# Optimization experiments

Hardware: AMD Instinct MI355X
Metric: run time of the kernel (lower is better)

The kernel has to match this reference:

```python
import jax, jax.numpy as jnp
import numpy as np

BSZ, T, L, D = 8, 8, 196, 192
E = D            # expand=1 -> d_inner
C = E * T        # d_inner_s = d_inner * d_t (scan channels)
N = 16           # d_state
K = 4            # d_conv
R = 96           # dt_rank = ceil(d_model*d_t/16)
DT_MIN, DT_MAX, DT_FLOOR = 1e-3, 1e-1, 1e-4


def setup_inputs() -> dict:
    key = jax.random.key(0)
    ks = jax.random.split(key, 9)
    hidden = jax.random.normal(ks[0], (BSZ, T, L, D), jnp.float32)
    in_proj_w = jax.random.normal(ks[1], (2 * E, D), jnp.float32) * (D ** -0.5)
    conv_w = jax.random.normal(ks[2], (C, K), jnp.float32) * 0.2
    conv_b = jax.random.normal(ks[3], (C,), jnp.float32) * 0.05
    x_proj_w = jax.random.normal(ks[4], (R + 2 * N, C), jnp.float32) * (C ** -0.5)
    dt_init_std = R ** -0.5
    dt_proj_w = jax.random.uniform(ks[5], (C, R), jnp.float32, -dt_init_std, dt_init_std)
    dt = jnp.exp(jax.random.uniform(ks[6], (C,), jnp.float32) * (np.log(DT_MAX) - np.log(DT_MIN)) + np.log(DT_MIN))
    dt = jnp.clip(dt, DT_FLOOR)
    dt_bias = dt + jnp.log(-jnp.expm1(-dt))  # inverse-softplus init
    A_log = jnp.log(jnp.tile(jnp.arange(1, N + 1, dtype=jnp.float32), (C, 1)))
    D_param = jnp.ones((C,), jnp.float32)
    return {"hidden": hidden, "in_proj_w": in_proj_w, "conv_w": conv_w, "conv_b": conv_b,
            "x_proj_w": x_proj_w, "dt_proj_w": dt_proj_w, "dt_bias": dt_bias,
            "A_log": A_log, "D_param": D_param}


def _silu(x):
    return x * jax.nn.sigmoid(x)


def reference(hidden, in_proj_w, conv_w, conv_b, x_proj_w, dt_proj_w, dt_bias, A_log, D_param):
    Bsz, T_, L_, D_ = hidden.shape
    E_ = in_proj_w.shape[0] // 2
    # in_proj (no bias): (B,T,L,D) @ (2E,D)^T -> (B,2E,T,L)
    xz = jnp.einsum('btld,ed->betl', hidden, in_proj_w)
    # rearrange 'b d t l -> b (d t) l' then chunk(2, dim=1)
    x = xz[:, :E_].reshape(Bsz, E_ * T_, L_)   # (B, C, L)
    z = xz[:, E_:].reshape(Bsz, E_ * T_, L_)
    # causal depthwise conv1d + silu
    x = jax.lax.conv_general_dilated(
        x, conv_w[:, None, :], window_strides=(1,), padding=[(K - 1, 0)],
        dimension_numbers=('NCH', 'OIH', 'NCH'), feature_group_count=conv_w.shape[0])
    x = _silu(x + conv_b[None, :, None])
    # x_proj -> dt, B, C
    x_dbl = jnp.einsum('bcl,rc->brl', x, x_proj_w)  # (B, R+2N, L)
    dt = x_dbl[:, :R]
    B_ssm = x_dbl[:, R:R + N]        # (B, N, L)
    C_ssm = x_dbl[:, R + N:]         # (B, N, L)
    delta = jax.nn.softplus(jnp.einsum('brl,cr->bcl', dt, dt_proj_w) + dt_bias[None, :, None])
    A = -jnp.exp(A_log)              # (C, N)
    # selective scan: h_l = exp(delta*A) * h_{l-1} + delta*B*x
    dA = jnp.exp(jnp.einsum('bcl,cn->lbcn', delta, A))       # (L,B,C,N)
    dBu = jnp.einsum('bcl,bnl,bcl->lbcn', delta, B_ssm, x)   # (L,B,C,N)

    def step(h, ab):
        a, b = ab
        h = h * a + b
        return h, h

    h0 = jnp.zeros((Bsz, dA.shape[2], dA.shape[3]), x.dtype)
    _, hs = jax.lax.scan(step, h0, (dA, dBu))                # (L,B,C,N)
    y = jnp.einsum('lbcn,bnl->bcl', hs, C_ssm)
    y = y + x * D_param[None, :, None]
    out = y * _silu(z)               # (B, C, L) — fused path output before out_proj
    return out
```

## Files before the change

### kernel.cpp

```cpp
#include <hip/hip_runtime.h>
#include <hip/hip_bf16.h>
#include <cstddef>

#define BSZ 8
#define T_  8
#define L_  196
#define D_  192
#define E_  192
#define C_  1536
#define N_  16
#define K_  4
#define R_  96

typedef __attribute__((ext_vector_type(8))) short short8;
typedef __attribute__((ext_vector_type(4))) float f32x4;
typedef unsigned short ushort_t;

__device__ __forceinline__ ushort_t f2bf(float x) {
  unsigned int bits = __float_as_uint(x);
  bits += 0x7FFFu + ((bits >> 16) & 1u);
  return (ushort_t)(bits >> 16);
}

__global__ __launch_bounds__(256) void k_cast_all(
    const float* __restrict__ hidden, const float* __restrict__ w,
    const float* __restrict__ wdt,
    ushort_t* __restrict__ hb, ushort_t* __restrict__ wb,
    ushort_t* __restrict__ wdtb) {
  const int H8 = 301056;
  const int W8 = H8 + 9216;
  const int T8 = W8 + 18432;
  int i = blockIdx.x * 256 + threadIdx.x;
  if (i >= T8) return;
  const float4* ip; uint4* op; int j;
  if (i < H8)      { ip = (const float4*)hidden; op = (uint4*)hb;   j = i; }
  else if (i < W8) { ip = (const float4*)w;      op = (uint4*)wb;   j = i - H8; }
  else             { ip = (const float4*)wdt;    op = (uint4*)wdtb; j = i - W8; }
  float4 v0 = ip[(size_t)j * 2];
  float4 v1 = ip[(size_t)j * 2 + 1];
  union { ushort_t u[8]; uint4 v; } r;
  float f[8] = {v0.x, v0.y, v0.z, v0.w, v1.x, v1.y, v1.z, v1.w};
#pragma unroll
  for (int k = 0; k < 8; k++) r.u[k] = f2bf(f[k]);
  op[j] = r.v;
}

__global__ __launch_bounds__(256) void k_inproj_mfma(
    const ushort_t* __restrict__ hb, const ushort_t* __restrict__ wb,
    float* __restrict__ xb, float* __restrict__ zb) {
  __shared__ float smem[64][97];
  int tid = threadIdx.x;
  int wave = tid >> 6, lane = tid & 63;
  int m0b = blockIdx.x * 64;
  int n0 = blockIdx.y * 96;
  int row = lane & 15, kg = lane >> 4;
  int m0w = m0b + wave * 16;

  f32x4 acc[6] = {};
  const ushort_t* ap = hb + (size_t)(m0w + row) * 192 + kg * 8;
#pragma unroll
  for (int ks = 0; ks < 6; ks++) {
    short8 a = *(const short8*)(ap + ks * 32);
#pragma unroll
    for (int nt = 0; nt < 6; nt++) {
      short8 b = *(const short8*)(wb + (size_t)(n0 + nt * 16 + row) * 192 + ks * 32 + kg * 8);
      acc[nt] = __builtin_amdgcn_mfma_f32_16x16x32_bf16(a, b, acc[nt], 0, 0, 0);
    }
  }
#pragma unroll
  for (int nt = 0; nt < 6; nt++) {
#pragma unroll
    for (int j = 0; j < 4; j++) {
      smem[wave * 16 + kg * 4 + j][nt * 16 + row] = acc[nt][j];
    }
  }
  __syncthreads();
  int mloc = tid & 63, eof = tid >> 6;
  int m_glob = m0b + mloc;
  int b = m_glob / 1568, u = m_glob % 1568;
  size_t obase = (size_t)b * 301056 + u;
#pragma unroll
  for (int e = eof; e < 96; e += 4) {
    int eg = n0 + e;
    float v = smem[mloc][e];
    if (eg < 192) xb[obase + (size_t)eg * 1568] = v;
    else          zb[obase + (size_t)(eg - 192) * 1568] = v;
  }
}

__global__ __launch_bounds__(256) void k_inproj_f32(
    const float* __restrict__ A, const float* __restrict__ W,
    float* __restrict__ xb, float* __restrict__ zb) {
  __shared__ float As[16][132];
  __shared__ float Bs[16][132];
  int tid = threadIdx.x;
  int m0 = blockIdx.x * 128;
  int n0 = blockIdx.y * 128;
  int tx = tid & 15, ty = tid >> 4;
  float acc[8][8] = {};
  for (int k0 = 0; k0 < 192; k0 += 16) {
#pragma unroll
    for (int i = 0; i < 2; i++) {
      int idx = tid + i * 256;
      int m = idx >> 2, k4 = (idx & 3) * 4;
      float4 v = *(const float4*)&A[(size_t)(m0 + m) * 192 + k0 + k4];
      As[k4 + 0][m] = v.x; As[k4 + 1][m] = v.y;
      As[k4 + 2][m] = v.z; As[k4 + 3][m] = v.w;
    }
#pragma unroll
    for (int i = 0; i < 2; i++) {
      int idx = tid + i * 256;
      int n = idx >> 2, k4 = (idx & 3) * 4;
      float4 v = *(const float4*)&W[(size_t)(n0 + n) * 192 + k0 + k4];
      Bs[k4 + 0][n] = v.x; Bs[k4 + 1][n] = v.y;
      Bs[k4 + 2][n] = v.z; Bs[k4 + 3][n] = v.w;
    }
    __syncthreads();
#pragma unroll
    for (int kk = 0; kk < 16; kk++) {
      float a_[8], b_[8];
      *(float4*)&a_[0] = *(const float4*)&As[kk][ty * 4];
      *(float4*)&a_[4] = *(const float4*)&As[kk][ty * 4 + 64];
      *(float4*)&b_[0] = *(const float4*)&Bs[kk][tx * 4];
      *(float4*)&b_[4] = *(const float4*)&Bs[kk][tx * 4 + 64];
#pragma unroll
      for (int i = 0; i < 8; i++)
#pragma unroll
        for (int j = 0; j < 8; j++) acc[i][j] += a_[i] * b_[j];
    }
    __syncthreads();
  }
#pragma unroll
  for (int i = 0; i < 8; i++) {
    int m = m0 + ty * 4 + (i & 3) + ((i >> 2) * 64);
    int b = m / (T_ * L_);
    int r = m % (T_ * L_);
    int t = r / L_;
    int l = r % L_;
#pragma unroll
    for (int j = 0; j < 8; j++) {
      int e = n0 + tx * 4 + (j & 3) + ((j >> 2) * 64);
      float v = acc[i][j];
      if (e < E_) {
        int c = e * T_ + t;
        xb[((size_t)b * C_ + c) * L_ + l] = v;
      } else {
        int c = (e - E_) * T_ + t;
        zb[((size_t)b * C_ + c) * L_ + l] = v;
      }
    }
  }
}

__global__ __launch_bounds__(256) void k_conv(
    const float* __restrict__ xb, const float* __restrict__ conv_w,
    const float* __restrict__ conv_b, float* __restrict__ xc) {
  int idx = blockIdx.x * 256 + threadIdx.x;
  int l = idx % L_;
  int bc = idx / L_;
  int c = bc % C_;
  const float* xrow = xb + (size_t)bc * L_;
  const float* w = conv_w + c * K_;
  float acc = conv_b[c];
#pragma unroll
  for (int k = 0; k < K_; k++) {
    int ll = l - (K_ - 1) + k;
    if (ll >= 0) acc += xrow[ll] * w[k];
  }
  xc[idx] = acc / (1.f + __expf(-acc));
}

#define XKK 32
__global__ __launch_bounds__(256) void k_xdbl_tile(
    const float* __restrict__ xb, const float* __restrict__ conv_w,
    const float* __restrict__ conv_b, const float* __restrict__ W,
    float* __restrict__ part, float* __restrict__ xcout) {
  __shared__ float Ws2[XKK][132];
  __shared__ float Xs[XKK][64];
  int tid = threadIdx.x;
  int n0 = blockIdx.x * 64;
  int c0 = blockIdx.y * 96;
  int tx = tid & 15, ty = tid >> 4;
  float acc[8][4] = {};
  for (int ck = 0; ck < 96; ck += XKK) {
#pragma unroll
    for (int p = 0; p < 4; p++) {
      int idx = tid + p * 256;
      int r = idx >> 3;
      int c4 = (idx & 7) * 4;
      float4 w4 = *(const float4*)&W[(size_t)r * 1536 + c0 + ck + c4];
      Ws2[c4 + 0][r] = w4.x; Ws2[c4 + 1][r] = w4.y;
      Ws2[c4 + 2][r] = w4.z; Ws2[c4 + 3][r] = w4.w;
    }
#pragma unroll
    for (int p = 0; p < 8; p++) {
      int idx = tid + p * 256;
      int c = idx >> 6, j = idx & 63;
      int n = n0 + j;
      float v = 0.f;
      if (n < BSZ * L_) {
        int b = n / L_, l = n - b * L_;
        int cc = c0 + ck + c;
        const float* row = xb + ((size_t)b * C_ + cc) * L_;
        float s = conv_b[cc];
#pragma unroll
        for (int k = 0; k < K_; k++) {
          int ll = l - 3 + k;
          if (ll >= 0) s += row[ll] * conv_w[cc * K_ + k];
        }
        v = s / (1.f + __expf(-s));
        xcout[((size_t)b * C_ + cc) * L_ + l] = v;
      }
      Xs[c][j] = v;
    }
    __syncthreads();
#pragma unroll
    for (int kk = 0; kk < XKK; kk++) {
      float w_[8], x_[4];
      *(float4*)&w_[0] = *(const float4*)&Ws2[kk][ty * 8];
      *(float4*)&w_[4] = *(const float4*)&Ws2[kk][ty * 8 + 4];
      *(float4*)&x_[0] = *(const float4*)&Xs[kk][tx * 4];
#pragma unroll
      for (int i = 0; i < 8; i++)
#pragma unroll
        for (int j = 0; j < 4; j++) acc[i][j] += w_[i] * x_[j];
    }
    __syncthreads();
  }
  int kc = blockIdx.y;
#pragma unroll
  for (int j = 0; j < 4; j++) {
    int n = n0 + tx * 4 + j;
    if (n < BSZ * L_) {
      int b = n / L_, l = n - b * L_;
      float* pp = &part[(((size_t)kc * 8 + b) * L_ + l) * 128 + ty * 8];
      float4 v0 = {acc[0][j], acc[1][j], acc[2][j], acc[3][j]};
      float4 v1 = {acc[4][j], acc[5][j], acc[6][j], acc[7][j]};
      *(float4*)&pp[0] = v0;
      *(float4*)&pp[4] = v1;
    }
  }
}

__global__ __launch_bounds__(256) void k_xreduce(
    const float* __restrict__ part, ushort_t* __restrict__ dtt,
    float* __restrict__ Bt, float* __restrict__ Ct) {
  int tx = threadIdx.x & 63;
  int ty = threadIdx.x >> 6;
  int l = blockIdx.x * 4 + ty;
  int b = blockIdx.y;
  size_t o = ((size_t)b * L_ + l) * 128 + tx;
  float v0 = 0.f, v1 = 0.f;
#pragma unroll
  for (int kc = 0; kc < 16; kc++) {
    v0 += part[(size_t)kc * (8 * L_ * 128) + o];
    v1 += part[(size_t)kc * (8 * L_ * 128) + o + 64];
  }
  int r1 = tx + 64;
  size_t nrow = ((size_t)b * L_ + l) * 96;
  dtt[nrow + tx] = f2bf(v0);
  if (r1 < 96) {
    dtt[nrow + r1] = f2bf(v1);
  } else if (r1 < 96 + N_) {
    Bt[((size_t)b * L_ + l) * N_ + (r1 - 96)] = v1;
  } else {
    Ct[((size_t)b * L_ + l) * N_ + (r1 - 96 - N_)] = v1;
  }
}

__global__ __launch_bounds__(256) void k_xdbl_mono(
    const float* __restrict__ xc, const float* __restrict__ W,
    float* __restrict__ xdbl, float* __restrict__ Bt, float* __restrict__ Ct) {
  int tx = threadIdx.x & 63;
  int ty = threadIdx.x >> 6;
  int l = blockIdx.x * 64 + tx;
  int r0 = blockIdx.y * 4 + ty;
  int r1 = r0 + 64;
  int b = blockIdx.z;
  if (l >= L_) return;
  const float* xcb = xc + (size_t)b * C_ * L_;
  float acc0 = 0.f, acc1 = 0.f;
#pragma unroll 4
  for (int c = 0; c < C_; c++) {
    float v = xcb[(size_t)c * L_ + l];
    acc0 += v * W[(size_t)r0 * C_ + c];
    acc1 += v * W[(size_t)r1 * C_ + c];
  }
  xdbl[((size_t)b * 96 + r0) * L_ + l] = acc0;
  if (r1 < 96) {
    xdbl[((size_t)b * 96 + r1) * L_ + l] = acc1;
  } else if (r1 < 96 + N_) {
    Bt[((size_t)b * L_ + l) * N_ + (r1 - 96)] = acc1;
  } else {
    Ct[((size_t)b * L_ + l) * N_ + (r1 - 96 - N_)] = acc1;
  }
}

__global__ __launch_bounds__(256) void k_delta_mfma(
    const ushort_t* __restrict__ wdtb,
    const ushort_t* __restrict__ dtt,
    const float* __restrict__ dt_bias, float* __restrict__ delta) {
  __shared__ float smem[64][65];
  int tid = threadIdx.x;
  int wave = tid >> 6, lane = tid & 63;
  int n0 = blockIdx.x * 64;
  int c0b = blockIdx.y * 64;
  int row = lane & 15, kg = lane >> 4;
  int c0w = c0b + wave * 16;
  f32x4 acc[4] = {};
  const ushort_t* ap = wdtb + (size_t)(c0w + row) * 96 + kg * 8;
#pragma unroll
  for (int ks = 0; ks < 3; ks++) {
    short8 a = *(const short8*)(ap + ks * 32);
#pragma unroll
    for (int nt = 0; nt < 4; nt++) {
      short8 b = *(const short8*)(dtt + (size_t)(n0 + nt * 16 + row) * 96 + ks * 32 + kg * 8);
      acc[nt] = __builtin_amdgcn_mfma_f32_16x16x32_bf16(a, b, acc[nt], 0, 0, 0);
    }
  }
#pragma unroll
  for (int nt = 0; nt < 4; nt++)
#pragma unroll
    for (int j = 0; j < 4; j++)
      smem[wave * 16 + kg * 4 + j][nt * 16 + row] = acc[nt][j];
  __syncthreads();
  int c_loc = tid >> 2, q = tid & 3;
  int c = c0b + c_loc;
  float bias = dt_bias[c];
#pragma unroll
  for (int i = 0; i < 16; i++) {
    int nn = n0 + q * 16 + i;
    if (nn < BSZ * L_) {
      int b = nn / L_, l = nn - b * L_;
      float v = smem[c_loc][q * 16 + i] + bias;
      float sp = (v > 20.f) ? v : __logf(1.f + __expf(v));
      delta[((size_t)b * C_ + c) * L_ + l] = sp;
    }
  }
}

__global__ __launch_bounds__(256) void k_delta_gemm(
    const float* __restrict__ dtm, const float* __restrict__ Wdt,
    const float* __restrict__ dt_bias, float* __restrict__ delta) {
  __shared__ float Ws[96][68];
  __shared__ float Ds[96][68];
  int tid = threadIdx.x;
  int n0 = blockIdx.x * 64;
  int c0 = blockIdx.y * 64;
  for (int idx = tid; idx < 64 * 96; idx += 256) {
    int i = idx / 96, r = idx - i * 96;
    Ws[r][i] = Wdt[(size_t)(c0 + i) * 96 + r];
  }
  for (int idx = tid; idx < 96 * 64; idx += 256) {
    int r = idx >> 6, j = idx & 63;
    int n = n0 + j;
    float v = 0.f;
    if (n < BSZ * L_) {
      int b = n / L_, l = n - b * L_;
      v = dtm[((size_t)b * 96 + r) * L_ + l];
    }
    Ds[r][j] = v;
  }
  __syncthreads();
  int tx = tid & 15, ty = tid >> 4;
  float acc[4][4] = {};
#pragma unroll 8
  for (int r = 0; r < 96; r++) {
    float4 av = *(const float4*)&Ws[r][ty * 4];
    float4 bv = *(const float4*)&Ds[r][tx * 4];
    float a_[4] = {av.x, av.y, av.z, av.w};
    float b_[4] = {bv.x, bv.y, bv.z, bv.w};
#pragma unroll
    for (int i = 0; i < 4; i++)
#pragma unroll
      for (int j = 0; j < 4; j++) acc[i][j] += a_[i] * b_[j];
  }
#pragma unroll
  for (int i = 0; i < 4; i++) {
    int c = c0 + ty * 4 + i;
    float bias = dt_bias[c];
#pragma unroll
    for (int j = 0; j < 4; j++) {
      int n = n0 + tx * 4 + j;
      if (n < BSZ * L_) {
        int b = n / L_, l = n - b * L_;
        float v = acc[i][j] + bias;
        float sp = (v > 20.f) ? v : __logf(1.f + __expf(v));
        delta[((size_t)b * C_ + c) * L_ + l] = sp;
      }
    }
  }
}

__global__ __launch_bounds__(512) void k_scan_fused(
    const float* __restrict__ delta, const float* __restrict__ xc,
    const float* __restrict__ zb, const float* __restrict__ Bt,
    const float* __restrict__ Ct, const float* __restrict__ A_log,
    const float* __restrict__ D_param, float* __restrict__ out) {
  __shared__ float BtS[196][20];
  __shared__ float CtS[196][20];
  __shared__ float yS[16][196];
  int tid = threadIdx.x;
  int b = blockIdx.y;
  int c_base = blockIdx.x * 16;
  int wave = tid >> 6, lane = tid & 63;
  int chunk = lane & 15;
  int nl = lane >> 4;
  bool act = chunk < 14;
  const int l0 = chunk * 14;
  int c0 = c_base + wave * 2;
  int c1 = c0 + 1;

  {
    const float4* gB = (const float4*)(Bt + (size_t)b * L_ * N_);
    const float4* gC = (const float4*)(Ct + (size_t)b * L_ * N_);
    for (int i = tid; i < 784; i += 512) {
      int l = i >> 2, q = i & 3;
      *(float4*)&BtS[l][q * 4] = gB[i];
      *(float4*)&CtS[l][q * 4] = gC[i];
    }
  }

  float4 a0, a1;
  {
    float4 t0 = *(const float4*)&A_log[c0 * N_ + nl * 4];
    float4 t1 = *(const float4*)&A_log[c1 * N_ + nl * 4];
    a0.x = -__expf(t0.x); a0.y = -__expf(t0.y);
    a0.z = -__expf(t0.z); a0.w = -__expf(t0.w);
    a1.x = -__expf(t1.x); a1.y = -__expf(t1.y);
    a1.z = -__expf(t1.z); a1.w = -__expf(t1.w);
  }
  size_t w0 = (size_t)(b * C_ + c0) * L_ + l0;
  size_t w1 = (size_t)(b * C_ + c1) * L_ + l0;

  float2 dv0[7], xv0[7], dv1[7], xv1[7];
  if (act) {
    const float2* d2a = (const float2*)(delta + w0);
    const float2* d2b = (const float2*)(delta + w1);
    const float2* x2a = (const float2*)(xc + w0);
    const float2* x2b = (const float2*)(xc + w1);
#pragma unroll
    for (int i = 0; i < 7; i++) {
      dv0[i] = d2a[i]; dv1[i] = d2b[i];
      xv0[i] = x2a[i]; xv1[i] = x2b[i];
    }
  } else {
#pragma unroll
    for (int i = 0; i < 7; i++) {
      dv0[i] = {0.f, 0.f}; dv1[i] = {0.f, 0.f};
      xv0[i] = {0.f, 0.f}; xv1[i] = {0.f, 0.f};
    }
  }
  __syncthreads();

  float4 h0 = {0.f,0.f,0.f,0.f}, p0 = {1.f,1.f,1.f,1.f};
  float4 h1 = {0.f,0.f,0.f,0.f}, p1 = {1.f,1.f,1.f,1.f};
#pragma unroll
  for (int l = 0; l < 14; l++) {
    float d0 = (l & 1) ? dv0[l >> 1].y : dv0[l >> 1].x;
    float d1 = (l & 1) ? dv1[l >> 1].y : dv1[l >> 1].x;
    float x0 = (l & 1) ? xv0[l >> 1].y : xv0[l >> 1].x;
    float x1 = (l & 1) ? xv1[l >> 1].y : xv1[l >> 1].x;
    float du0 = d0 * x0, du1 = d1 * x1;
    float4 Bv = *(const float4*)&BtS[l0 + l][nl * 4];
    float e0x = __expf(d0 * a0.x), e0y = __expf(d0 * a0.y);
    float e0z = __expf(d0 * a0.z), e0w = __expf(d0 * a0.w);
    float e1x = __expf(d1 * a1.x), e1y = __expf(d1 * a1.y);
    float e1z = __expf(d1 * a1.z), e1w = __expf(d1 * a1.w);
    h0.x = h0.x * e0x + du0 * Bv.x; p0.x *= e0x;
    h0.y = h0.y * e0y + du0 * Bv.y; p0.y *= e0y;
    h0.z = h0.z * e0z + du0 * Bv.z; p0.z *= e0z;
    h0.w = h0.w * e0w + du0 * Bv.w; p0.w *= e0w;
    h1.x = h1.x * e1x + du1 * Bv.x; p1.x *= e1x;
    h1.y = h1.y * e1y + du1 * Bv.y; p1.y *= e1y;
    h1.z = h1.z * e1z + du1 * Bv.z; p1.z *= e1z;
    h1.w = h1.w * e1w + du1 * Bv.w; p1.w *= e1w;
  }

#pragma unroll
  for (int s = 1; s < 16; s <<= 1) {
    float4 P0, Q0, P1, Q1;
    P0.x = __shfl_up(p0.x, s, 16); Q0.x = __shfl_up(h0.x, s, 16);
    P0.y = __shfl_up(p0.y, s, 16); Q0.y = __shfl_up(h0.y, s, 16);
    P0.z = __shfl_up(p0.z, s, 16); Q0.z = __shfl_up(h0.z, s, 16);
    P0.w = __shfl_up(p0.w, s, 16); Q0.w = __shfl_up(h0.w, s, 16);
    P1.x = __shfl_up(p1.x, s, 16); Q1.x = __shfl_up(h1.x, s, 16);
    P1.y = __shfl_up(p1.y, s, 16); Q1.y = __shfl_up(h1.y, s, 16);
    P1.z = __shfl_up(p1.z, s, 16); Q1.z = __shfl_up(h1.z, s, 16);
    P1.w = __shfl_up(p1.w, s, 16); Q1.w = __shfl_up(h1.w, s, 16);
    if (chunk >= s) {
      h0.x = p0.x * Q0.x + h0.x; p0.x *= P0.x;
      h0.y = p0.y * Q0.y + h0.y; p0.y *= P0.y;
      h0.z = p0.z * Q0.z + h0.z; p0.z *= P0.z;
      h0.w = p0.w * Q0.w + h0.w; p0.w *= P0.w;
      h1.x = p1.x * Q1.x + h1.x; p1.x *= P1.x;
      h1.y = p1.y * Q1.y + h1.y; p1.y *= P1.y;
      h1.z = p1.z * Q1.z + h1.z; p1.z *= P1.z;
      h1.w = p1.w * Q1.w + h1.w; p1.w *= P1.w;
    }
  }
  float4 g0, g1;
  g0.x = __shfl_up(h0.x, 1, 16); g1.x = __shfl_up(h1.x, 1, 16);
  g0.y = __shfl_up(h0.y, 1, 16); g1.y = __shfl_up(h1.y, 1, 16);
  g0.z = __shfl_up(h0.z, 1, 16); g1.z = __shfl_up(h1.z, 1, 16);
  g0.w = __shfl_up(h0.w, 1, 16); g1.w = __shfl_up(h1.w, 1, 16);
  if (chunk == 0) {
    g0.x = g0.y = g0.z = g0.w = 0.f;
    g1.x = g1.y = g1.z = g1.w = 0.f;
  }

  if (act) {
#pragma unroll
    for (int l = 0; l < 14; l++) {
      float d0 = (l & 1) ? dv0[l >> 1].y : dv0[l >> 1].x;
      float d1 = (l & 1) ? dv1[l >> 1].y : dv1[l >> 1].x;
      float x0 = (l & 1) ? xv0[l >> 1].y : xv0[l >> 1].x;
      float x1 = (l & 1) ? xv1[l >> 1].y : xv1[l >> 1].x;
      float du0 = d0 * x0, du1 = d1 * x1;
      float4 Bv = *(const float4*)&BtS[l0 + l][nl * 4];
      float4 Cv = *(const float4*)&CtS[l0 + l][nl * 4];
      float e0x = __expf(d0 * a0.x), e0y = __expf(d0 * a0.y);
      float e0z = __expf(d0 * a0.z), e0w = __expf(d0 * a0.w);
      float e1x = __expf(d1 * a1.x), e1y = __expf(d1 * a1.y);
      float e1z = __expf(d1 * a1.z), e1w = __expf(d1 * a1.w);
      g0.x = g0.x * e0x + du0 * Bv.x;
      g0.y = g0.y * e0y + du0 * Bv.y;
      g0.z = g0.z * e0z + du0 * Bv.z;
      g0.w = g0.w * e0w + du0 * Bv.w;
      g1.x = g1.x * e1x + du1 * Bv.x;
      g1.y = g1.y * e1y + du1 * Bv.y;
      g1.z = g1.z * e1z + du1 * Bv.z;
      g1.w = g1.w * e1w + du1 * Bv.w;
      float y0 = g0.x * Cv.x + g0.y * Cv.y + g0.z * Cv.z + g0.w * Cv.w;
      float y1 = g1.x * Cv.x + g1.y * Cv.y + g1.z * Cv.z + g1.w * Cv.w;
      y0 += __shfl_xor(y0, 16);
      y0 += __shfl_xor(y0, 32);
      y1 += __shfl_xor(y1, 16);
      y1 += __shfl_xor(y1, 32);
      if (nl == 0) {
        yS[wave * 2 + 0][l0 + l] = y0;
        yS[wave * 2 + 1][l0 + l] = y1;
      }
    }
  }
  __syncthreads();

  size_t base = (size_t)(b * C_ + c_base) * L_;
  for (int idx = tid; idx < 16 * L_; idx += 512) {
    int cloc = idx / L_, l = idx - cloc * L_;
    float y = yS[cloc][l];
    float xv = xc[base + idx];
    float zv = zb[base + idx];
    float Dp = D_param[c_base + cloc];
    float sz = zv / (1.f + __expf(-zv));
    out[base + idx] = (y + xv * Dp) * sz;
  }
}

extern "C" void kernel_launch(void* const* d_in, const int* in_sizes, int n_in,
                              void* d_out, int out_size, void* d_ws, size_t ws_size,
                              hipStream_t stream) {
  const float* hidden    = (const float*)d_in[0];
  const float* in_proj_w = (const float*)d_in[1];
  const float* conv_w    = (const float*)d_in[2];
  const float* conv_b    = (const float*)d_in[3];
  const float* x_proj_w  = (const float*)d_in[4];
  const float* dt_proj_w = (const float*)d_in[5];
  const float* dt_bias   = (const float*)d_in[6];
  const float* A_log     = (const float*)d_in[7];
  const float* D_param   = (const float*)d_in[8];
  float* out = (float*)d_out;

  const size_t NBCL   = (size_t)BSZ * C_ * L_;
  const size_t NBT    = (size_t)BSZ * L_ * N_;
  const size_t NDT    = (size_t)BSZ * 96 * L_;
  const size_t NPART  = (size_t)16 * BSZ * L_ * 128;
  const size_t NHID   = (size_t)BSZ * T_ * L_ * D_;
  const size_t NW1    = (size_t)2 * E_ * D_;
  const size_t NDTTF  = 76800;
  const size_t NWDTF  = 73728;
  float* ws = (float*)d_ws;
  float* xb    = ws;
  float* zb    = xb + NBCL;
  float* xc    = zb + NBCL;
  float* BtArr = xc + NBCL;
  float* CtArr = BtArr + NBT;
  float* dttF  = CtArr + NBT;
  float* wdtbF = dttF + NDTTF;
  float* Pbuf  = wdtbF + NWDTF;
  float* delta = xb;

  size_t need = 3 * NBCL + 2 * NBT + NDTTF + NWDTF + NPART;
  bool split_ok = ws_size / 4 >= need;

  if (split_ok) {
    ushort_t* hb   = (ushort_t*)Pbuf;
    ushort_t* wb   = hb + NHID;
    ushort_t* wdtb = (ushort_t*)wdtbF;
    ushort_t* dtt  = (ushort_t*)dttF;
    float* part = Pbuf;

    k_cast_all<<<1284, 256, 0, stream>>>(hidden, in_proj_w, dt_proj_w, hb, wb, wdtb);
    k_inproj_mfma<<<dim3(196, 4), 256, 0, stream>>>(hb, wb, xb, zb);
    k_xdbl_tile<<<dim3(25, 16), 256, 0, stream>>>(xb, conv_w, conv_b, x_proj_w, part, xc);
    k_xreduce<<<dim3(49, BSZ), 256, 0, stream>>>(part, dtt, BtArr, CtArr);
    k_delta_mfma<<<dim3(25, 24), 256, 0, stream>>>(wdtb, dtt, dt_bias, delta);
    k_scan_fused<<<dim3(C_ / 16, BSZ), 512, 0, stream>>>(delta, xc, zb, BtArr, CtArr,
                                                         A_log, D_param, out);
  } else {
    float* xdblF = Pbuf;
    k_inproj_f32<<<dim3(98, 3), 256, 0, stream>>>(hidden, in_proj_w, xb, zb);
    k_conv<<<(int)(NBCL / 256), 256, 0, stream>>>(xb, conv_w, conv_b, xc);
    k_xdbl_mono<<<dim3(4, 16, BSZ), 256, 0, stream>>>(xc, x_proj_w, xdblF, BtArr, CtArr);
    k_delta_gemm<<<dim3(25, 24), 256, 0, stream>>>(xdblF, dt_proj_w, dt_bias, delta);
    k_scan_fused<<<dim3(C_ / 16, BSZ), 512, 0, stream>>>(delta, xc, zb, BtArr, CtArr,
                                                         A_log, D_param, out);
  }
}
```

Baseline: 119.8 us.

## Replace fp32 split-K x_proj GEMM with bf16 MFMA and conv-cast kernel

Splits the fused conv+x_proj tile kernel into a conv+SiLU kernel that also writes a transposed bf16 copy of the activations, followed by a bf16 MFMA GEMM over the full 1536-wide reduction. This removes the split-K partial buffer and its separate reduction kernel, and moves the x_proj work from FP32 FMA onto matrix cores. The x_proj weight is now cast to bf16 in the existing cast kernel. The cost is an extra bf16 activation buffer and lower precision in the dt/B/C projections. The MFMA kernel launches only 200 blocks, each running a serial 48-step reduction.

```diff
diff --git a/kernel.cpp b/kernel.cpp
--- a/kernel.cpp
+++ b/kernel.cpp
@@ -24,18 +24,20 @@
 
 __global__ __launch_bounds__(256) void k_cast_all(
     const float* __restrict__ hidden, const float* __restrict__ w,
-    const float* __restrict__ wdt,
+    const float* __restrict__ wdt, const float* __restrict__ wx,
     ushort_t* __restrict__ hb, ushort_t* __restrict__ wb,
-    ushort_t* __restrict__ wdtb) {
+    ushort_t* __restrict__ wdtb, ushort_t* __restrict__ wxb) {
   const int H8 = 301056;
   const int W8 = H8 + 9216;
-  const int T8 = W8 + 18432;
+  const int D8 = W8 + 18432;
+  const int T8 = D8 + 24576;
   int i = blockIdx.x * 256 + threadIdx.x;
   if (i >= T8) return;
   const float4* ip; uint4* op; int j;
   if (i < H8)      { ip = (const float4*)hidden; op = (uint4*)hb;   j = i; }
   else if (i < W8) { ip = (const float4*)w;      op = (uint4*)wb;   j = i - H8; }
-  else             { ip = (const float4*)wdt;    op = (uint4*)wdtb; j = i - W8; }
+  else if (i < D8) { ip = (const float4*)wdt;    op = (uint4*)wdtb; j = i - W8; }
+  else             { ip = (const float4*)wx;     op = (uint4*)wxb;  j = i - D8; }
   float4 v0 = ip[(size_t)j * 2];
   float4 v1 = ip[(size_t)j * 2 + 1];
   union { ushort_t u[8]; uint4 v; } r;
@@ -152,6 +154,48 @@
   }
 }
 
+__global__ __launch_bounds__(256) void k_conv_cast(
+    const float* __restrict__ xb, const float* __restrict__ conv_w,
+    const float* __restrict__ conv_b, float* __restrict__ xc,
+    ushort_t* __restrict__ xcb) {
+  __shared__ float sm[64][33];
+  int tid = threadIdx.x;
+  int l0 = blockIdx.x * 32;
+  int c0 = blockIdx.y * 64;
+  int b  = blockIdx.z;
+  int c_loc = tid >> 2, lq = tid & 3;
+  int c = c0 + c_loc;
+  const float* xrow = xb + ((size_t)b * C_ + c) * L_;
+  float* xcrow = xc + ((size_t)b * C_ + c) * L_;
+  float w0 = conv_w[c * K_ + 0], w1 = conv_w[c * K_ + 1];
+  float w2 = conv_w[c * K_ + 2], w3 = conv_w[c * K_ + 3];
+  float cb = conv_b[c];
+#pragma unroll
+  for (int i = 0; i < 8; i++) {
+    int l = l0 + lq * 8 + i;
+    if (l < L_) {
+      float s = cb;
+      if (l >= 3) s += xrow[l - 3] * w0;
+      if (l >= 2) s += xrow[l - 2] * w1;
+      if (l >= 1) s += xrow[l - 1] * w2;
+      s += xrow[l] * w3;
+      float v = s / (1.f + __expf(-s));
+      xcrow[l] = v;
+      sm[c_loc][lq * 8 + i] = v;
+    }
+  }
+  __syncthreads();
+  int l_loc = tid >> 3, cg = tid & 7;
+  int l = l0 + l_loc;
+  if (l < L_) {
+    int n = b * L_ + l;
+    union { ushort_t u[8]; uint4 v; } r;
+#pragma unroll
+    for (int i = 0; i < 8; i++) r.u[i] = f2bf(sm[cg * 8 + i][l_loc]);
+    *(uint4*)&xcb[(size_t)n * 1536 + c0 + cg * 8] = r.v;
+  }
+}
+
 __global__ __launch_bounds__(256) void k_conv(
     const float* __restrict__ xb, const float* __restrict__ conv_w,
     const float* __restrict__ conv_b, float* __restrict__ xc) {
@@ -170,101 +214,42 @@
   xc[idx] = acc / (1.f + __expf(-acc));
 }
 
-#define XKK 32
-__global__ __launch_bounds__(256) void k_xdbl_tile(
-    const float* __restrict__ xb, const float* __restrict__ conv_w,
-    const float* __restrict__ conv_b, const float* __restrict__ W,
-    float* __restrict__ part, float* __restrict__ xcout) {
-  __shared__ float Ws2[XKK][132];
-  __shared__ float Xs[XKK][64];
+__global__ __launch_bounds__(256) void k_xdbl_mfma(
+    const ushort_t* __restrict__ wxb,
+    const ushort_t* __restrict__ xcb,
+    ushort_t* __restrict__ dtt,
+    float* __restrict__ Bt, float* __restrict__ Ct) {
+  __shared__ float sm[16][68];
   int tid = threadIdx.x;
+  int wave = tid >> 6, lane = tid & 63;
   int n0 = blockIdx.x * 64;
-  int c0 = blockIdx.y * 96;
-  int tx = tid & 15, ty = tid >> 4;
-  float acc[8][4] = {};
-  for (int ck = 0; ck < 96; ck += XKK) {
-#pragma unroll
-    for (int p = 0; p < 4; p++) {
-      int idx = tid + p * 256;
-      int r = idx >> 3;
-      int c4 = (idx & 7) * 4;
-      float4 w4 = *(const float4*)&W[(size_t)r * 1536 + c0 + ck + c4];
-      Ws2[c4 + 0][r] = w4.x; Ws2[c4 + 1][r] = w4.y;
-      Ws2[c4 + 2][r] = w4.z; Ws2[c4 + 3][r] = w4.w;
-    }
-#pragma unroll
-    for (int p = 0; p < 8; p++) {
-      int idx = tid + p * 256;
-      int c = idx >> 6, j = idx & 63;
-      int n = n0 + j;
-      float v = 0.f;
-      if (n < BSZ * L_) {
-        int b = n / L_, l = n - b * L_;
-        int cc = c0 + ck + c;
-        const float* row = xb + ((size_t)b * C_ + cc) * L_;
-        float s = conv_b[cc];
-#pragma unroll
-        for (int k = 0; k < K_; k++) {
-          int ll = l - 3 + k;
-          if (ll >= 0) s += row[ll] * conv_w[cc * K_ + k];
-        }
-        v = s / (1.f + __expf(-s));
-        xcout[((size_t)b * C_ + cc) * L_ + l] = v;
-      }
-      Xs[c][j] = v;
-    }
-    __syncthreads();
-#pragma unroll
-    for (int kk = 0; kk < XKK; kk++) {
-      float w_[8], x_[4];
-      *(float4*)&w_[0] = *(const float4*)&Ws2[kk][ty * 8];
-      *(float4*)&w_[4] = *(const float4*)&Ws2[kk][ty * 8 + 4];
-      *(float4*)&x_[0] = *(const float4*)&Xs[kk][tx * 4];
-#pragma unroll
-      for (int i = 0; i < 8; i++)
-#pragma unroll
-        for (int j = 0; j < 4; j++) acc[i][j] += w_[i] * x_[j];
-    }
-    __syncthreads();
-  }
-  int kc = blockIdx.y;
-#pragma unroll
-  for (int j = 0; j < 4; j++) {
-    int n = n0 + tx * 4 + j;
-    if (n < BSZ * L_) {
-      int b = n / L_, l = n - b * L_;
-      float* pp = &part[(((size_t)kc * 8 + b) * L_ + l) * 128 + ty * 8];
-      float4 v0 = {acc[0][j], acc[1][j], acc[2][j], acc[3][j]};
-      float4 v1 = {acc[4][j], acc[5][j], acc[6][j], acc[7][j]};
-      *(float4*)&pp[0] = v0;
-      *(float4*)&pp[4] = v1;
-    }
-  }
-}
-
-__global__ __launch_bounds__(256) void k_xreduce(
-    const float* __restrict__ part, ushort_t* __restrict__ dtt,
-    float* __restrict__ Bt, float* __restrict__ Ct) {
-  int tx = threadIdx.x & 63;
-  int ty = threadIdx.x >> 6;
-  int l = blockIdx.x * 4 + ty;
-  int b = blockIdx.y;
-  size_t o = ((size_t)b * L_ + l) * 128 + tx;
-  float v0 = 0.f, v1 = 0.f;
-#pragma unroll
-  for (int kc = 0; kc < 16; kc++) {
-    v0 += part[(size_t)kc * (8 * L_ * 128) + o];
-    v1 += part[(size_t)kc * (8 * L_ * 128) + o + 64];
-  }
-  int r1 = tx + 64;
-  size_t nrow = ((size_t)b * L_ + l) * 96;
-  dtt[nrow + tx] = f2bf(v0);
-  if (r1 < 96) {
-    dtt[nrow + r1] = f2bf(v1);
-  } else if (r1 < 96 + N_) {
-    Bt[((size_t)b * L_ + l) * N_ + (r1 - 96)] = v1;
-  } else {
-    Ct[((size_t)b * L_ + l) * N_ + (r1 - 96 - N_)] = v1;
+  int m0 = blockIdx.y * 16;
+  int row = lane & 15, kg = lane >> 4;
+  f32x4 acc = {};
+  const ushort_t* ap = wxb + (size_t)(m0 + row) * 1536 + kg * 8;
+  const ushort_t* bp = xcb + (size_t)(n0 + wave * 16 + row) * 1536 + kg * 8;
+#pragma unroll 8
+  for (int ks = 0; ks < 48; ks++) {
+    short8 a = *(const short8*)(ap + ks * 32);
+    short8 b = *(const short8*)(bp + ks * 32);
+    acc = __builtin_amdgcn_mfma_f32_16x16x32_bf16(a, b, acc, 0, 0, 0);
+  }
+#pragma unroll
+  for (int j = 0; j < 4; j++)
+    sm[kg * 4 + j][wave * 16 + row] = acc[j];
+  __syncthreads();
+  int n_loc = tid >> 2, mg = tid & 3;
+  int n = n0 + n_loc;
+  if (m0 < 96) {
+    union { ushort_t u[4]; uint2 v; } r;
+#pragma unroll
+    for (int j = 0; j < 4; j++) r.u[j] = f2bf(sm[mg * 4 + j][n_loc]);
+    *(uint2*)&dtt[(size_t)n * 96 + m0 + mg * 4] = r.v;
+  } else if (n < BSZ * L_) {
+    float4 v = {sm[mg * 4 + 0][n_loc], sm[mg * 4 + 1][n_loc],
+                sm[mg * 4 + 2][n_loc], sm[mg * 4 + 3][n_loc]};
+    float* dst = (m0 == 96) ? Bt : Ct;
+    *(float4*)&dst[(size_t)n * 16 + mg * 4] = v;
   }
 }
 
@@ -278,11 +263,11 @@
   int r1 = r0 + 64;
   int b = blockIdx.z;
   if (l >= L_) return;
-  const float* xcb = xc + (size_t)b * C_ * L_;
+  const float* xcb2 = xc + (size_t)b * C_ * L_;
   float acc0 = 0.f, acc1 = 0.f;
 #pragma unroll 4
   for (int c = 0; c < C_; c++) {
-    float v = xcb[(size_t)c * L_ + l];
+    float v = xcb2[(size_t)c * L_ + l];
     acc0 += v * W[(size_t)r0 * C_ + c];
     acc1 += v * W[(size_t)r1 * C_ + c];
   }
@@ -573,12 +558,13 @@
 
   const size_t NBCL   = (size_t)BSZ * C_ * L_;
   const size_t NBT    = (size_t)BSZ * L_ * N_;
-  const size_t NDT    = (size_t)BSZ * 96 * L_;
-  const size_t NPART  = (size_t)16 * BSZ * L_ * 128;
   const size_t NHID   = (size_t)BSZ * T_ * L_ * D_;
   const size_t NW1    = (size_t)2 * E_ * D_;
   const size_t NDTTF  = 76800;
   const size_t NWDTF  = 73728;
+  const size_t NWXF   = 98304;
+  const size_t NXCBF  = 1228800;
+  const size_t NCASTF = (NHID + NW1) / 2;
   float* ws = (float*)d_ws;
   float* xb    = ws;
   float* zb    = xb + NBCL;
@@ -587,23 +573,27 @@
   float* CtArr = BtArr + NBT;
   float* dttF  = CtArr + NBT;
   float* wdtbF = dttF + NDTTF;
-  float* Pbuf  = wdtbF + NWDTF;
+  float* wxbF  = wdtbF + NWDTF;
+  float* xcbF  = wxbF + NWXF;
+  float* Pbuf  = xcbF + NXCBF;
   float* delta = xb;
 
-  size_t need = 3 * NBCL + 2 * NBT + NDTTF + NWDTF + NPART;
+  size_t need = 3 * NBCL + 2 * NBT + NDTTF + NWDTF + NWXF + NXCBF + NCASTF;
   bool split_ok = ws_size / 4 >= need;
 
   if (split_ok) {
     ushort_t* hb   = (ushort_t*)Pbuf;
     ushort_t* wb   = hb + NHID;
     ushort_t* wdtb = (ushort_t*)wdtbF;
+    ushort_t* wxb  = (ushort_t*)wxbF;
     ushort_t* dtt  = (ushort_t*)dttF;
-    float* part = Pbuf;
-
-    k_cast_all<<<1284, 256, 0, stream>>>(hidden, in_proj_w, dt_proj_w, hb, wb, wdtb);
+    ushort_t* xcb  = (ushort_t*)xcbF;
+
+    k_cast_all<<<1380, 256, 0, stream>>>(hidden, in_proj_w, dt_proj_w, x_proj_w,
+                                         hb, wb, wdtb, wxb);
     k_inproj_mfma<<<dim3(196, 4), 256, 0, stream>>>(hb, wb, xb, zb);
-    k_xdbl_tile<<<dim3(25, 16), 256, 0, stream>>>(xb, conv_w, conv_b, x_proj_w, part, xc);
-    k_xreduce<<<dim3(49, BSZ), 256, 0, stream>>>(part, dtt, BtArr, CtArr);
+    k_conv_cast<<<dim3(7, 24, BSZ), 256, 0, stream>>>(xb, conv_w, conv_b, xc, xcb);
+    k_xdbl_mfma<<<dim3(25, 8), 256, 0, stream>>>(wxb, xcb, dtt, BtArr, CtArr);
     k_delta_mfma<<<dim3(25, 24), 256, 0, stream>>>(wdtb, dtt, dt_bias, delta);
     k_scan_fused<<<dim3(C_ / 16, BSZ), 512, 0, stream>>>(delta, xc, zb, BtArr, CtArr,
                                                          A_log, D_param, out);
```

Result: slower. 133.5 us (+11.4%).

## Fuse dt_proj MFMA GEMM and softplus into scan kernel via shared memory

Applied to the files above, without the earlier changes.

Removes the separate delta GEMM kernel and computes delta for each scan block's 16 channels inside the scan kernel with bf16 MFMA, storing the softplus result in shared memory. This avoids writing and re-reading the full B*C*L delta tensor through global memory and saves one launch. The price is extra shared memory and MFMA work at the start of the scan kernel, which may lower occupancy. The fallback path keeps the old behaviour in a copied kernel, k_scan_f32.

```diff
diff --git a/kernel.cpp b/kernel.cpp
--- a/kernel.cpp
+++ b/kernel.cpp
@@ -296,49 +296,6 @@
   }
 }
 
-__global__ __launch_bounds__(256) void k_delta_mfma(
-    const ushort_t* __restrict__ wdtb,
-    const ushort_t* __restrict__ dtt,
-    const float* __restrict__ dt_bias, float* __restrict__ delta) {
-  __shared__ float smem[64][65];
-  int tid = threadIdx.x;
-  int wave = tid >> 6, lane = tid & 63;
-  int n0 = blockIdx.x * 64;
-  int c0b = blockIdx.y * 64;
-  int row = lane & 15, kg = lane >> 4;
-  int c0w = c0b + wave * 16;
-  f32x4 acc[4] = {};
-  const ushort_t* ap = wdtb + (size_t)(c0w + row) * 96 + kg * 8;
-#pragma unroll
-  for (int ks = 0; ks < 3; ks++) {
-    short8 a = *(const short8*)(ap + ks * 32);
-#pragma unroll
-    for (int nt = 0; nt < 4; nt++) {
-      short8 b = *(const short8*)(dtt + (size_t)(n0 + nt * 16 + row) * 96 + ks * 32 + kg * 8);
-      acc[nt] = __builtin_amdgcn_mfma_f32_16x16x32_bf16(a, b, acc[nt], 0, 0, 0);
-    }
-  }
-#pragma unroll
-  for (int nt = 0; nt < 4; nt++)
-#pragma unroll
-    for (int j = 0; j < 4; j++)
-      smem[wave * 16 + kg * 4 + j][nt * 16 + row] = acc[nt][j];
-  __syncthreads();
-  int c_loc = tid >> 2, q = tid & 3;
-  int c = c0b + c_loc;
-  float bias = dt_bias[c];
-#pragma unroll
-  for (int i = 0; i < 16; i++) {
-    int nn = n0 + q * 16 + i;
-    if (nn < BSZ * L_) {
-      int b = nn / L_, l = nn - b * L_;
-      float v = smem[c_loc][q * 16 + i] + bias;
-      float sp = (v > 20.f) ? v : __logf(1.f + __expf(v));
-      delta[((size_t)b * C_ + c) * L_ + l] = sp;
-    }
-  }
-}
-
 __global__ __launch_bounds__(256) void k_delta_gemm(
     const float* __restrict__ dtm, const float* __restrict__ Wdt,
     const float* __restrict__ dt_bias, float* __restrict__ delta) {
@@ -393,13 +350,16 @@
 }
 
 __global__ __launch_bounds__(512) void k_scan_fused(
-    const float* __restrict__ delta, const float* __restrict__ xc,
-    const float* __restrict__ zb, const float* __restrict__ Bt,
-    const float* __restrict__ Ct, const float* __restrict__ A_log,
-    const float* __restrict__ D_param, float* __restrict__ out) {
+    const float* __restrict__ xc, const float* __restrict__ zb,
+    const float* __restrict__ Bt, const float* __restrict__ Ct,
+    const float* __restrict__ A_log, const float* __restrict__ D_param,
+    const ushort_t* __restrict__ wdtb,
+    const ushort_t* __restrict__ dtt,
+    const float* __restrict__ dt_bias, float* __restrict__ out) {
   __shared__ float BtS[196][20];
   __shared__ float CtS[196][20];
   __shared__ float yS[16][196];
+  __shared__ float dS[16][200];
   int tid = threadIdx.x;
   int b = blockIdx.y;
   int c_base = blockIdx.x * 16;
@@ -421,6 +381,29 @@
     }
   }
 
+  {
+    const ushort_t* ap2 = wdtb + (size_t)(c_base + chunk) * 96 + nl * 8;
+    for (int nt = wave; nt < 13; nt += 8) {
+      f32x4 accd = {};
+      const ushort_t* bp2 = dtt + (size_t)(b * L_ + nt * 16 + chunk) * 96 + nl * 8;
+#pragma unroll
+      for (int ks = 0; ks < 3; ks++) {
+        short8 a = *(const short8*)(ap2 + ks * 32);
+        short8 bb = *(const short8*)(bp2 + ks * 32);
+        accd = __builtin_amdgcn_mfma_f32_16x16x32_bf16(a, bb, accd, 0, 0, 0);
+      }
+      int lcol = nt * 16 + chunk;
+#pragma unroll
+      for (int j = 0; j < 4; j++) {
+        int c_loc = nl * 4 + j;
+        if (lcol < L_) {
+          float v = accd[j] + dt_bias[c_base + c_loc];
+          dS[c_loc][lcol] = (v > 20.f) ? v : __logf(1.f + __expf(v));
+        }
+      }
+    }
+  }
+
   float4 a0, a1;
   {
     float4 t0 = *(const float4*)&A_log[c0 * N_ + nl * 4];
@@ -433,25 +416,29 @@
   size_t w0 = (size_t)(b * C_ + c0) * L_ + l0;
   size_t w1 = (size_t)(b * C_ + c1) * L_ + l0;
 
-  float2 dv0[7], xv0[7], dv1[7], xv1[7];
+  float2 xv0[7], xv1[7];
   if (act) {
-    const float2* d2a = (const float2*)(delta + w0);
-    const float2* d2b = (const float2*)(delta + w1);
     const float2* x2a = (const float2*)(xc + w0);
     const float2* x2b = (const float2*)(xc + w1);
 #pragma unroll
+    for (int i = 0; i < 7; i++) { xv0[i] = x2a[i]; xv1[i] = x2b[i]; }
+  } else {
+#pragma unroll
+    for (int i = 0; i < 7; i++) { xv0[i] = {0.f, 0.f}; xv1[i] = {0.f, 0.f}; }
+  }
+  __syncthreads();
+
+  float2 dv0[7], dv1[7];
+  if (act) {
+#pragma unroll
     for (int i = 0; i < 7; i++) {
-      dv0[i] = d2a[i]; dv1[i] = d2b[i];
-      xv0[i] = x2a[i]; xv1[i] = x2b[i];
+      dv0[i] = *(const float2*)&dS[wave * 2 + 0][l0 + 2 * i];
+      dv1[i] = *(const float2*)&dS[wave * 2 + 1][l0 + 2 * i];
     }
   } else {
 #pragma unroll
-    for (int i = 0; i < 7; i++) {
-      dv0[i] = {0.f, 0.f}; dv1[i] = {0.f, 0.f};
-      xv0[i] = {0.f, 0.f}; xv1[i] = {0.f, 0.f};
-    }
-  }
-  __syncthreads();
+    for (int i = 0; i < 7; i++) { dv0[i] = {0.f, 0.f}; dv1[i] = {0.f, 0.f}; }
+  }
 
   float4 h0 = {0.f,0.f,0.f,0.f}, p0 = {1.f,1.f,1.f,1.f};
   float4 h1 = {0.f,0.f,0.f,0.f}, p1 = {1.f,1.f,1.f,1.f};
@@ -557,6 +544,164 @@
   }
 }
 
+__global__ __launch_bounds__(512) void k_scan_f32(
+    const float* __restrict__ delta, const float* __restrict__ xc,
+    const float* __restrict__ zb, const float* __restrict__ Bt,
+    const float* __restrict__ Ct, const float* __restrict__ A_log,
+    const float* __restrict__ D_param, float* __restrict__ out) {
+  __shared__ float BtS[196][20];
+  __shared__ float CtS[196][20];
+  __shared__ float yS[16][196];
+  int tid = threadIdx.x;
+  int b = blockIdx.y;
+  int c_base = blockIdx.x * 16;
+  int wave = tid >> 6, lane = tid & 63;
+  int chunk = lane & 15;
+  int nl = lane >> 4;
+  bool act = chunk < 14;
+  const int l0 = chunk * 14;
+  int c0 = c_base + wave * 2;
+  int c1 = c0 + 1;
+  {
+    const float4* gB = (const float4*)(Bt + (size_t)b * L_ * N_);
+    const float4* gC = (const float4*)(Ct + (size_t)b * L_ * N_);
+    for (int i = tid; i < 784; i += 512) {
+      int l = i >> 2, q = i & 3;
+      *(float4*)&BtS[l][q * 4] = gB[i];
+      *(float4*)&CtS[l][q * 4] = gC[i];
+    }
+  }
+  float4 a0, a1;
+  {
+    float4 t0 = *(const float4*)&A_log[c0 * N_ + nl * 4];
+    float4 t1 = *(const float4*)&A_log[c1 * N_ + nl * 4];
+    a0.x = -__expf(t0.x); a0.y = -__expf(t0.y);
+    a0.z = -__expf(t0.z); a0.w = -__expf(t0.w);
+    a1.x = -__expf(t1.x); a1.y = -__expf(t1.y);
+    a1.z = -__expf(t1.z); a1.w = -__expf(t1.w);
+  }
+  size_t w0 = (size_t)(b * C_ + c0) * L_ + l0;
+  size_t w1 = (size_t)(b * C_ + c1) * L_ + l0;
+  float2 dv0[7], xv0[7], dv1[7], xv1[7];
+  if (act) {
+    const float2* d2a = (const float2*)(delta + w0);
+    const float2* d2b = (const float2*)(delta + w1);
+    const float2* x2a = (const float2*)(xc + w0);
+    const float2* x2b = (const float2*)(xc + w1);
+#pragma unroll
+    for (int i = 0; i < 7; i++) {
+      dv0[i] = d2a[i]; dv1[i] = d2b[i];
+      xv0[i] = x2a[i]; xv1[i] = x2b[i];
+    }
+  } else {
+#pragma unroll
+    for (int i = 0; i < 7; i++) {
+      dv0[i] = {0.f, 0.f}; dv1[i] = {0.f, 0.f};
+      xv0[i] = {0.f, 0.f}; xv1[i] = {0.f, 0.f};
+    }
+  }
+  __syncthreads();
+  float4 h0 = {0.f,0.f,0.f,0.f}, p0 = {1.f,1.f,1.f,1.f};
+  float4 h1 = {0.f,0.f,0.f,0.f}, p1 = {1.f,1.f,1.f,1.f};
+#pragma unroll
+  for (int l = 0; l < 14; l++) {
+    float d0 = (l & 1) ? dv0[l >> 1].y : dv0[l >> 1].x;
+    float d1 = (l & 1) ? dv1[l >> 1].y : dv1[l >> 1].x;
+    float x0 = (l & 1) ? xv0[l >> 1].y : xv0[l >> 1].x;
+    float x1 = (l & 1) ? xv1[l >> 1].y : xv1[l >> 1].x;
+    float du0 = d0 * x0, du1 = d1 * x1;
+    float4 Bv = *(const float4*)&BtS[l0 + l][nl * 4];
+    float e0x = __expf(d0 * a0.x), e0y = __expf(d0 * a0.y);
+    float e0z = __expf(d0 * a0.z), e0w = __expf(d0 * a0.w);
+    float e1x = __expf(d1 * a1.x), e1y = __expf(d1 * a1.y);
+    float e1z = __expf(d1 * a1.z), e1w = __expf(d1 * a1.w);
+    h0.x = h0.x * e0x + du0 * Bv.x; p0.x *= e0x;
+    h0.y = h0.y * e0y + du0 * Bv.y; p0.y *= e0y;
+    h0.z = h0.z * e0z + du0 * Bv.z; p0.z *= e0z;
+    h0.w = h0.w * e0w + du0 * Bv.w; p0.w *= e0w;
+    h1.x = h1.x * e1x + du1 * Bv.x; p1.x *= e1x;
+    h1.y = h1.y * e1y + du1 * Bv.y; p1.y *= e1y;
+    h1.z = h1.z * e1z + du1 * Bv.z; p1.z *= e1z;
+    h1.w = h1.w * e1w + du1 * Bv.w; p1.w *= e1w;
+  }
+#pragma unroll
+  for (int s = 1; s < 16; s <<= 1) {
+    float4 P0, Q0, P1, Q1;
+    P0.x = __shfl_up(p0.x, s, 16); Q0.x = __shfl_up(h0.x, s, 16);
+    P0.y = __shfl_up(p0.y, s, 16); Q0.y = __shfl_up(h0.y, s, 16);
+    P0.z = __shfl_up(p0.z, s, 16); Q0.z = __shfl_up(h0.z, s, 16);
+    P0.w = __shfl_up(p0.w, s, 16); Q0.w = __shfl_up(h0.w, s, 16);
+    P1.x = __shfl_up(p1.x, s, 16); Q1.x = __shfl_up(h1.x, s, 16);
+    P1.y = __shfl_up(p1.y, s, 16); Q1.y = __shfl_up(h1.y, s, 16);
+    P1.z = __shfl_up(p1.z, s, 16); Q1.z = __shfl_up(h1.z, s, 16);
+    P1.w = __shfl_up(p1.w, s, 16); Q1.w = __shfl_up(h1.w, s, 16);
+    if (chunk >= s) {
+      h0.x = p0.x * Q0.x + h0.x; p0.x *= P0.x;
+      h0.y = p0.y * Q0.y + h0.y; p0.y *= P0.y;
+      h0.z = p0.z * Q0.z + h0.z; p0.z *= P0.z;
+      h0.w = p0.w * Q0.w + h0.w; p0.w *= P0.w;
+      h1.x = p1.x * Q1.x + h1.x; p1.x *= P1.x;
+      h1.y = p1.y * Q1.y + h1.y; p1.y *= P1.y;
+      h1.z = p1.z * Q1.z + h1.z; p1.z *= P1.z;
+      h1.w = p1.w * Q1.w + h1.w; p1.w *= P1.w;
+    }
+  }
+  float4 g0, g1;
+  g0.x = __shfl_up(h0.x, 1, 16); g1.x = __shfl_up(h1.x, 1, 16);
+  g0.y = __shfl_up(h0.y, 1, 16); g1.y = __shfl_up(h1.y, 1, 16);
+  g0.z = __shfl_up(h0.z, 1, 16); g1.z = __shfl_up(h1.z, 1, 16);
+  g0.w = __shfl_up(h0.w, 1, 16); g1.w = __shfl_up(h1.w, 1, 16);
+  if (chunk == 0) {
+    g0.x = g0.y = g0.z = g0.w = 0.f;
+    g1.x = g1.y = g1.z = g1.w = 0.f;
+  }
+  if (act) {
+#pragma unroll
+    for (int l = 0; l < 14; l++) {
+      float d0 = (l & 1) ? dv0[l >> 1].y : dv0[l >> 1].x;
+      float d1 = (l & 1) ? dv1[l >> 1].y : dv1[l >> 1].x;
+      float x0 = (l & 1) ? xv0[l >> 1].y : xv0[l >> 1].x;
+      float x1 = (l & 1) ? xv1[l >> 1].y : xv1[l >> 1].x;
+      float du0 = d0 * x0, du1 = d1 * x1;
+      float4 Bv = *(const float4*)&BtS[l0 + l][nl * 4];
+      float4 Cv = *(const float4*)&CtS[l0 + l][nl * 4];
+      float e0x = __expf(d0 * a0.x), e0y = __expf(d0 * a0.y);
+      float e0z = __expf(d0 * a0.z), e0w = __expf(d0 * a0.w);
+      float e1x = __expf(d1 * a1.x), e1y = __expf(d1 * a1.y);
+      float e1z = __expf(d1 * a1.z), e1w = __expf(d1 * a1.w);
+      g0.x = g0.x * e0x + du0 * Bv.x;
+      g0.y = g0.y * e0y + du0 * Bv.y;
+      g0.z = g0.z * e0z + du0 * Bv.z;
+      g0.w = g0.w * e0w + du0 * Bv.w;
+      g1.x = g1.x * e1x + du1 * Bv.x;
+      g1.y = g1.y * e1y + du1 * Bv.y;
+      g1.z = g1.z * e1z + du1 * Bv.z;
+      g1.w = g1.w * e1w + du1 * Bv.w;
+      float y0 = g0.x * Cv.x + g0.y * Cv.y + g0.z * Cv.z + g0.w * Cv.w;
+      float y1 = g1.x * Cv.x + g1.y * Cv.y + g1.z * Cv.z + g1.w * Cv.w;
+      y0 += __shfl_xor(y0, 16);
+      y0 += __shfl_xor(y0, 32);
+      y1 += __shfl_xor(y1, 16);
+      y1 += __shfl_xor(y1, 32);
+      if (nl == 0) {
+        yS[wave * 2 + 0][l0 + l] = y0;
+        yS[wave * 2 + 1][l0 + l] = y1;
+      }
+    }
+  }
+  __syncthreads();
+  size_t base = (size_t)(b * C_ + c_base) * L_;
+  for (int idx = tid; idx < 16 * L_; idx += 512) {
+    int cloc = idx / L_, l = idx - cloc * L_;
+    float y = yS[cloc][l];
+    float xv = xc[base + idx];
+    float zv = zb[base + idx];
+    float Dp = D_param[c_base + cloc];
+    float sz = zv / (1.f + __expf(-zv));
+    out[base + idx] = (y + xv * Dp) * sz;
+  }
+}
+
 extern "C" void kernel_launch(void* const* d_in, const int* in_sizes, int n_in,
                               void* d_out, int out_size, void* d_ws, size_t ws_size,
                               hipStream_t stream) {
@@ -573,10 +718,8 @@
 
   const size_t NBCL   = (size_t)BSZ * C_ * L_;
   const size_t NBT    = (size_t)BSZ * L_ * N_;
-  const size_t NDT    = (size_t)BSZ * 96 * L_;
   const size_t NPART  = (size_t)16 * BSZ * L_ * 128;
   const size_t NHID   = (size_t)BSZ * T_ * L_ * D_;
-  const size_t NW1    = (size_t)2 * E_ * D_;
   const size_t NDTTF  = 76800;
   const size_t NWDTF  = 73728;
   float* ws = (float*)d_ws;
@@ -604,16 +747,16 @@
     k_inproj_mfma<<<dim3(196, 4), 256, 0, stream>>>(hb, wb, xb, zb);
     k_xdbl_tile<<<dim3(25, 16), 256, 0, stream>>>(xb, conv_w, conv_b, x_proj_w, part, xc);
     k_xreduce<<<dim3(49, BSZ), 256, 0, stream>>>(part, dtt, BtArr, CtArr);
-    k_delta_mfma<<<dim3(25, 24), 256, 0, stream>>>(wdtb, dtt, dt_bias, delta);
-    k_scan_fused<<<dim3(C_ / 16, BSZ), 512, 0, stream>>>(delta, xc, zb, BtArr, CtArr,
-                                                         A_log, D_param, out);
+    k_scan_fused<<<dim3(C_ / 16, BSZ), 512, 0, stream>>>(xc, zb, BtArr, CtArr,
+                                                         A_log, D_param,
+                                                         wdtb, dtt, dt_bias, out);
   } else {
     float* xdblF = Pbuf;
     k_inproj_f32<<<dim3(98, 3), 256, 0, stream>>>(hidden, in_proj_w, xb, zb);
     k_conv<<<(int)(NBCL / 256), 256, 0, stream>>>(xb, conv_w, conv_b, xc);
     k_xdbl_mono<<<dim3(4, 16, BSZ), 256, 0, stream>>>(xc, x_proj_w, xdblF, BtArr, CtArr);
     k_delta_gemm<<<dim3(25, 24), 256, 0, stream>>>(xdblF, dt_proj_w, dt_bias, delta);
-    k_scan_fused<<<dim3(C_ / 16, BSZ), 512, 0, stream>>>(delta, xc, zb, BtArr, CtArr,
-                                                         A_log, D_param, out);
-  }
-}
+    k_scan_f32<<<dim3(C_ / 16, BSZ), 512, 0, stream>>>(delta, xc, zb, BtArr, CtArr,
+                                                       A_log, D_param, out);
+  }
+}
```

After: 107.1 us, median of 3. 10.6% less time.
